# Performance work log

Measured on AMD Instinct MI355X. Metric: run time of the kernel, lower is better.

The kernel has to match this reference:

```python
import jax, jax.numpy as jnp
import numpy as np

B, T, C, H = 4, 1024, 1024, 16
D = C // H


def setup_inputs() -> dict:
    key = jax.random.key(0)
    ks = jax.random.split(key, 6)
    s = 1.0 / np.sqrt(C)
    return {
        "x": jax.random.normal(ks[0], (B, T, C), jnp.float32),
        "W_qkv": jax.random.normal(ks[1], (C, 3 * C), jnp.float32) * s,
        "b_qkv": jnp.zeros((3 * C,), jnp.float32),
        "W_out": jax.random.normal(ks[2], (C, C), jnp.float32) * s,
        "b_out": jnp.zeros((C,), jnp.float32),
        "w_sur": jax.random.normal(ks[3], (C,), jnp.float32) * s,
        "b_sur": jnp.zeros((), jnp.float32),
        "threshold": jnp.float32(0.5),
    }


def _expmap0_split(u):
    # geoopt Lorentz (k=1) expmap0: first coordinate is the time axis.
    # Minkowski norm of tangent u: sqrt(clamp(-u0^2 + |u_rest|^2, 1e-8))
    mink = -u[..., :1] ** 2 + jnp.sum(u[..., 1:] ** 2, axis=-1, keepdims=True)
    nomin = jnp.sqrt(jnp.maximum(mink, 1e-8))  # [..., 1]
    time = jnp.cosh(nomin)                      # [..., 1]
    space = jnp.sinh(nomin) * u[..., 1:] / nomin  # [..., D-1]
    return time, space


def reference(x, W_qkv, b_qkv, W_out, b_out, w_sur, b_sur, threshold):
    Bx, Tx, Cx = x.shape
    # spiking gate on query rows (causal tril over a (T,1) matrix is all-True -> no-op)
    importance = jax.nn.sigmoid(jnp.einsum("btc,c->bt", x, w_sur) + b_sur)  # [B,T]
    spikes = (importance > threshold).astype(x.dtype)                       # [B,T]
    spike_mask = spikes[:, None, :, None]                                   # [B,1,T,1]

    qkv = x @ W_qkv + b_qkv                                                 # [B,T,3C]
    qkv = qkv.reshape(Bx, Tx, 3, H, D).transpose(2, 0, 3, 1, 4)             # [3,B,H,T,D]
    q, k, v = qkv[0], qkv[1], qkv[2]

    tq, sq = _expmap0_split(q)  # [B,H,T,1], [B,H,T,D-1]
    tk, sk = _expmap0_split(k)
    # -<x,y>_L = tq*tk - <sq,sk>  (pairwise, via matmuls instead of broadcast tensors)
    neg_inner = jnp.einsum("bhie,bhje->bhij", tq, tk) - jnp.einsum(
        "bhid,bhjd->bhij", sq, sk
    )  # [B,H,T,T]
    dist = jnp.arccosh(jnp.maximum(neg_inner, 1.0 + 1e-7))
    scores = -(dist ** 2) / np.sqrt(D)

    causal = jnp.tril(jnp.ones((Tx, Tx), dtype=bool))
    scores = jnp.where(causal[None, None], scores, -jnp.inf)
    attn = jax.nn.softmax(scores, axis=-1) * spike_mask                     # [B,H,T,T]

    y = jnp.einsum("bhij,bhjd->bhid", attn, v)                              # [B,H,T,D]
    y = y.transpose(0, 2, 1, 3).reshape(Bx, Tx, Cx)
    return y @ W_out + b_out
```

## Files before the change

### kernel.cpp

```cpp
#include <hip/hip_runtime.h>
#include <math.h>

#define BB 4
#define TT 1024
#define CC 1024
#define HH 16
#define DD 64
#define NQKV (3 * CC)
#define MROWS (BB * TT)

typedef __attribute__((ext_vector_type(8))) short bf16x8;
typedef __attribute__((ext_vector_type(4))) float f32x4;

struct alignas(8) US4 { unsigned short x, y, z, w; };

__device__ __forceinline__ float b2f(unsigned short u) {
  unsigned int w = ((unsigned int)u) << 16;
  float f; __builtin_memcpy(&f, &w, 4); return f;
}
__device__ __forceinline__ unsigned short f2b(float f) {
  unsigned int u; __builtin_memcpy(&u, &f, 4);
  u += 0x7FFFu + ((u >> 16) & 1);
  return (unsigned short)(u >> 16);
}

__device__ __forceinline__ float hw_log2(float x) {
  return __builtin_amdgcn_logf(x);
}
__device__ __forceinline__ float hw_exp2(float x) {
  return __builtin_amdgcn_exp2f(x);
}

__device__ __forceinline__ void gload16(const void* g, void* l) {
  __builtin_amdgcn_global_load_lds(
      (const __attribute__((address_space(1))) unsigned int*)g,
      (__attribute__((address_space(3))) unsigned int*)l, 16, 0, 0);
}

__device__ __forceinline__ bf16x8 ld_sw(const unsigned short* row_base,
                                        int lc, int rsw) {
  return *(const bf16x8*)((const char*)row_base + (((lc ^ rsw) & 7) << 4));
}

__global__ __launch_bounds__(256) void prep(
    const float* __restrict__ x, const float* __restrict__ w_sur,
    const float* __restrict__ b_sur, const float* __restrict__ thr,
    const float* __restrict__ W_qkv, const float* __restrict__ W_out,
    float* __restrict__ spikes, unsigned short* __restrict__ xb,
    unsigned short* __restrict__ WqkvT, unsigned short* __restrict__ WoutT) {
  __shared__ float t[32][33];
  const int blk = blockIdx.x;

  if (blk < 4096) {
    const float* W; unsigned short* WT; int K, N, bx, by;
    if (blk < 3072) {
      W = W_qkv; WT = WqkvT; K = CC; N = NQKV;
      bx = blk % 96; by = blk / 96;
    } else {
      W = W_out; WT = WoutT; K = CC; N = CC;
      const int b2 = blk - 3072;
      bx = b2 & 31; by = b2 >> 5;
    }
    const int tx = threadIdx.x & 31, ty = threadIdx.x >> 5;
    const int k0 = by * 32, n0 = bx * 32;
#pragma unroll
    for (int i = 0; i < 32; i += 8)
      t[ty + i][tx] = W[(size_t)(k0 + ty + i) * N + n0 + tx];
    __syncthreads();
#pragma unroll
    for (int i = 0; i < 32; i += 8)
      WT[(size_t)(n0 + ty + i) * K + k0 + tx] = f2b(t[tx][ty + i]);
  } else {
    const int row = (blk - 4096) * 4 + (threadIdx.x >> 6);
    const int lane = threadIdx.x & 63;
    const float* xr = x + (size_t)row * CC;
    unsigned short* xo = xb + (size_t)row * CC;
    double acc = 0.0;
#pragma unroll
    for (int s = 0; s < 4; ++s) {
      const int idx = s * 256 + lane * 4;
      const float4 xv = *(const float4*)(xr + idx);
      const float4 wv = *(const float4*)(w_sur + idx);
      acc += (double)xv.x * (double)wv.x;
      acc += (double)xv.y * (double)wv.y;
      acc += (double)xv.z * (double)wv.z;
      acc += (double)xv.w * (double)wv.w;
      US4 o = {f2b(xv.x), f2b(xv.y), f2b(xv.z), f2b(xv.w)};
      *(US4*)(xo + idx) = o;
    }
#pragma unroll
    for (int off = 32; off > 0; off >>= 1) acc += __shfl_xor(acc, off, 64);
    if (lane == 0) {
      const float z = (float)acc + b_sur[0];
      const float imp = 1.0f / (1.0f + __expf(-z));
      spikes[row] = (imp > thr[0]) ? 1.0f : 0.0f;
    }
  }
}

__global__ __launch_bounds__(256, 3) void gemm_qkv(
    const unsigned short* __restrict__ A, const unsigned short* __restrict__ BT,
    const float* __restrict__ bias, unsigned short* __restrict__ qkvb,
    unsigned short* __restrict__ vT) {
  const int K = CC;
  __shared__ unsigned short SH[16384];
  unsigned short (*As)[64] = (unsigned short(*)[64])SH;
  unsigned short (*Bs)[64] = (unsigned short(*)[64])(SH + 8192);
  const int tid = threadIdx.x;
  const int lane = tid & 63;
  const int wave = tid >> 6;
  const int wr = wave >> 1;
  const int wc = wave & 1;
  const int m0 = blockIdx.y * 128;
  const int n0 = blockIdx.x * 128;
  const int ln15 = lane & 15;
  const int g = lane >> 4;
  const int rsw = ln15 & 7;

  const int srow = tid >> 3;
  const int schk = ((tid & 7) ^ (srow & 7)) * 8;
  const unsigned short* gA = A + (size_t)(m0 + srow) * K + schk;
  const unsigned short* gB = BT + (size_t)(n0 + srow) * K + schk;
  char* lA = (char*)SH + wave * 1024;
  char* lB = (char*)SH + 16384 + wave * 1024;

  f32x4 acc[4][4] = {};

  for (int k0 = 0; k0 < K; k0 += 64) {
    __syncthreads();
#pragma unroll
    for (int i = 0; i < 4; ++i)
      gload16(gA + k0 + (size_t)(32 * i) * K, lA + i * 4096);
#pragma unroll
    for (int i = 0; i < 4; ++i)
      gload16(gB + k0 + (size_t)(32 * i) * K, lB + i * 4096);
    __syncthreads();

#pragma unroll
    for (int c = 0; c < 2; ++c) {
      bf16x8 af[4], bfr[4];
#pragma unroll
      for (int i = 0; i < 4; ++i)
        af[i] = ld_sw(&As[wr * 64 + i * 16 + ln15][0], c * 4 + g, rsw);
#pragma unroll
      for (int j = 0; j < 4; ++j)
        bfr[j] = ld_sw(&Bs[wc * 64 + j * 16 + ln15][0], c * 4 + g, rsw);
#pragma unroll
      for (int i = 0; i < 4; ++i)
#pragma unroll
        for (int j = 0; j < 4; ++j)
          acc[i][j] = __builtin_amdgcn_mfma_f32_16x16x32_bf16(
              af[i], bfr[j], acc[i][j], 0, 0, 0);
    }
  }

  __syncthreads();
  unsigned short* scr = SH + wave * 4096;

  const int bx = blockIdx.x;
  if (bx < 16) {
    const bool isk = (bx >= 8);
#pragma unroll
    for (int i = 0; i < 4; ++i) {
#pragma unroll
      for (int r = 0; r < 4; ++r) {
        float u[4];
        float part = 0.f;
#pragma unroll
        for (int j = 0; j < 4; ++j) {
          u[j] = acc[i][j][r] + bias[n0 + wc * 64 + j * 16 + ln15];
          float sq = u[j] * u[j];
          if (j == 0 && ln15 == 0) sq = -sq;
          part += sq;
        }
#pragma unroll
        for (int off = 1; off < 16; off <<= 1)
          part += __shfl_xor(part, off, 64);
        const float nomin = sqrtf(fmaxf(part, 1e-8f));
        const float e = __expf(nomin);
        const float ei = __builtin_amdgcn_rcpf(e);
        const float tim = 0.5f * (e + ei);
        const float coef = 0.5f * (e - ei) * __builtin_amdgcn_rcpf(nomin);
        const int lrow = i * 16 + g * 4 + r;
#pragma unroll
        for (int j = 0; j < 4; ++j) {
          float o = (j == 0 && ln15 == 0) ? tim : coef * u[j];
          if (isk && !(j == 0 && ln15 == 0)) o = -o;
          const int col = j * 16 + ln15;
          const int ch = ((col >> 3) + lrow) & 7;
          scr[lrow * 64 + ch * 8 + (col & 7)] = f2b(o);
        }
      }
    }
#pragma unroll
    for (int it = 0; it < 8; ++it) {
      const int row = (lane >> 3) + 8 * it;
      const int ch = lane & 7;
      const int ph = (ch + row) & 7;
      const bf16x8 v = *(const bf16x8*)&scr[row * 64 + ph * 8];
      *(bf16x8*)&qkvb[(size_t)(m0 + wr * 64 + row) * NQKV + n0 + wc * 64 + ch * 8] = v;
    }
  } else {
#pragma unroll
    for (int i = 0; i < 4; ++i) {
#pragma unroll
      for (int j = 0; j < 4; ++j) {
        const float bb_ = bias[n0 + wc * 64 + j * 16 + ln15];
        const int drow = j * 16 + ln15;
#pragma unroll
        for (int r = 0; r < 4; ++r) {
          const int col = i * 16 + g * 4 + r;
          const int ch = ((col >> 3) + drow) & 7;
          scr[drow * 64 + ch * 8 + (col & 7)] = f2b(acc[i][j][r] + bb_);
        }
      }
    }
    const int hh = (bx - 16) * 2 + wc;
    const int mbase = m0 + wr * 64;
    const int bq = mbase >> 10;
    const int t0 = mbase & 1023;
#pragma unroll
    for (int it = 0; it < 8; ++it) {
      const int drow = (lane >> 3) + 8 * it;
      const int ch = lane & 7;
      const int ph = (ch + drow) & 7;
      const bf16x8 v = *(const bf16x8*)&scr[drow * 64 + ph * 8];
      *(bf16x8*)&vT[((size_t)(bq * HH + hh) * DD + drow) * TT + t0 + ch * 8] = v;
    }
  }
}

__global__ __launch_bounds__(256) void gemm_out(
    const unsigned short* __restrict__ A, const unsigned short* __restrict__ BT,
    const float* __restrict__ bias, float* __restrict__ C) {
  const int N = CC, K = CC;
  __shared__ unsigned short As[128][64];
  __shared__ unsigned short Bs[64][64];
  const int tid = threadIdx.x;
  const int lane = tid & 63;
  const int wave = tid >> 6;
  const int wm = wave * 32;
  const int m0 = blockIdx.y * 128;
  const int n0 = blockIdx.x * 64;
  const int ln15 = lane & 15;
  const int g = lane >> 4;
  const int rsw = ln15 & 7;

  const int srow = tid >> 3;
  const int schk = ((tid & 7) ^ (srow & 7)) * 8;
  const unsigned short* gA = A + (size_t)(m0 + srow) * K + schk;
  const unsigned short* gB = BT + (size_t)(n0 + srow) * K + schk;
  char* lA = (char*)As + wave * 1024;
  char* lB = (char*)Bs + wave * 1024;

  f32x4 acc[2][4] = {};

  for (int k0 = 0; k0 < K; k0 += 64) {
    __syncthreads();
#pragma unroll
    for (int i = 0; i < 4; ++i)
      gload16(gA + k0 + (size_t)(32 * i) * K, lA + i * 4096);
#pragma unroll
    for (int i = 0; i < 2; ++i)
      gload16(gB + k0 + (size_t)(32 * i) * K, lB + i * 4096);
    __syncthreads();

#pragma unroll
    for (int c = 0; c < 2; ++c) {
      bf16x8 af[2], bfr[4];
#pragma unroll
      for (int i = 0; i < 2; ++i)
        af[i] = ld_sw(&As[wm + i * 16 + ln15][0], c * 4 + g, rsw);
#pragma unroll
      for (int j = 0; j < 4; ++j)
        bfr[j] = ld_sw(&Bs[j * 16 + ln15][0], c * 4 + g, rsw);
#pragma unroll
      for (int i = 0; i < 2; ++i)
#pragma unroll
        for (int j = 0; j < 4; ++j)
          acc[i][j] = __builtin_amdgcn_mfma_f32_16x16x32_bf16(
              af[i], bfr[j], acc[i][j], 0, 0, 0);
    }
  }

#pragma unroll
  for (int i = 0; i < 2; ++i) {
#pragma unroll
    for (int r = 0; r < 4; ++r) {
      const int m = m0 + wm + i * 16 + g * 4 + r;
#pragma unroll
      for (int j = 0; j < 4; ++j) {
        const int n = n0 + j * 16 + ln15;
        C[(size_t)m * N + n] = acc[i][j][r] + bias[n];
      }
    }
  }
}

__global__ __launch_bounds__(512) void flash_mfma(
    const unsigned short* __restrict__ qkv, const unsigned short* __restrict__ vT,
    const float* __restrict__ spikes, unsigned short* __restrict__ y) {
  __shared__ unsigned short Ks[128][68];
  __shared__ unsigned short Vs[64][136];
  __shared__ unsigned short Ps[128][68];

  const int tid = threadIdx.x;
  const int lane = tid & 63;
  const int wave = tid >> 6;
  const int ln15 = lane & 15;
  const int g = lane >> 4;
  const int bh = blockIdx.y;
  const int itile = (bh < 32) ? ((int)gridDim.x - 1 - (int)blockIdx.x)
                              : (int)blockIdx.x;
  const int b = bh >> 4;
  const int h = bh & 15;
  const int i0 = itile * 128;
  const int band = wave * 16;
  const int htiles = itile + 1;
  const unsigned short* base = qkv + (size_t)b * TT * NQKV;
  const unsigned short* vbase = vT + (size_t)bh * DD * TT;
  const int qoff = h * DD;
  const int koff = CC + h * DD;

  const int ksn = tid >> 2;
  const int kqc = (tid & 3) * 2;
  const int vsn = tid >> 3;
  const int vqc = (tid & 7) * 2;

  bf16x8 qf[2];
  {
    const unsigned short* qp = base + (size_t)(i0 + band + ln15) * NQKV + qoff;
    qf[0] = *(const bf16x8*)(qp + g * 8);
    qf[1] = *(const bf16x8*)(qp + 32 + g * 8);
  }

  f32x4 accy[4] = {};
  float lrow[4] = {0.f, 0.f, 0.f, 0.f};

  float4 kr0, kr1, vr0, vr1;
  {
    const unsigned short* kp = base + (size_t)ksn * NQKV + koff + kqc * 8;
    const unsigned short* vp = vbase + (size_t)vsn * TT + vqc * 8;
    kr0 = *(const float4*)(kp + 0);
    kr1 = *(const float4*)(kp + 8);
    vr0 = *(const float4*)(vp + 0);
    vr1 = *(const float4*)(vp + 8);
  }

  for (int ht = 0; ht < htiles; ++ht) {
    const int j0h = ht * 128;
    __syncthreads();
    *(float4*)&Ks[ksn][kqc * 8 + 0] = kr0;
    *(float4*)&Ks[ksn][kqc * 8 + 8] = kr1;
    *(float4*)&Vs[vsn][vqc * 8 + 0] = vr0;
    *(float4*)&Vs[vsn][vqc * 8 + 8] = vr1;
    __syncthreads();

    if (ht + 1 < htiles) {
      const int j1 = j0h + 128;
      const unsigned short* kp = base + (size_t)(j1 + ksn) * NQKV + koff + kqc * 8;
      const unsigned short* vp = vbase + (size_t)vsn * TT + j1 + vqc * 8;
      kr0 = *(const float4*)(kp + 0);
      kr1 = *(const float4*)(kp + 8);
      vr0 = *(const float4*)(vp + 0);
      vr1 = *(const float4*)(vp + 8);
    }

#pragma unroll
    for (int t2 = 0; t2 < 2; ++t2) {
      const int j0 = j0h + t2 * 64;
      if (j0 > i0 + band + 15) continue;

      f32x4 sf[4];
#pragma unroll
      for (int j = 0; j < 4; ++j) {
        const bf16x8 k0 = *(const bf16x8*)&Ks[t2 * 64 + j * 16 + ln15][g * 8];
        const bf16x8 k1 = *(const bf16x8*)&Ks[t2 * 64 + j * 16 + ln15][32 + g * 8];
        f32x4 z = {};
        z = __builtin_amdgcn_mfma_f32_16x16x32_bf16(qf[0], k0, z, 0, 0, 0);
        sf[j] = __builtin_amdgcn_mfma_f32_16x16x32_bf16(qf[1], k1, z, 0, 0, 0);
      }

      float p[4][4];
      if (j0 + 63 <= i0 + band) {
#pragma unroll
        for (int j = 0; j < 4; ++j)
#pragma unroll
          for (int r = 0; r < 4; ++r) {
            const float l = hw_log2(fmaxf(sf[j][r], 1.0f));
            const float s = l + 1.0f;
            p[r][j] = hw_exp2(-0.08664339757f * s * s);
          }
      } else {
#pragma unroll
        for (int j = 0; j < 4; ++j) {
          const int gj = j0 + j * 16 + ln15;
#pragma unroll
          for (int r = 0; r < 4; ++r) {
            const int gi = i0 + band + g * 4 + r;
            float e;
            if (gj > gi) {
              e = 0.f;
            } else {
              const float l = hw_log2(fmaxf(sf[j][r], 1.0f));
              const float s = l + 1.0f;
              e = hw_exp2(-0.08664339757f * s * s);
            }
            p[r][j] = e;
          }
        }
      }
#pragma unroll
      for (int r = 0; r < 4; ++r)
        lrow[r] += (p[r][0] + p[r][1]) + (p[r][2] + p[r][3]);

#pragma unroll
      for (int r = 0; r < 4; ++r)
#pragma unroll
        for (int j = 0; j < 4; ++j)
          Ps[band + g * 4 + r][j * 16 + ln15] = f2b(p[r][j]);

      const bf16x8 pa0 = *(const bf16x8*)&Ps[band + ln15][g * 8];
      const bf16x8 pa1 = *(const bf16x8*)&Ps[band + ln15][32 + g * 8];
#pragma unroll
      for (int dt = 0; dt < 4; ++dt) {
        const bf16x8 v0 = *(const bf16x8*)&Vs[dt * 16 + ln15][t2 * 64 + g * 8];
        const bf16x8 v1 = *(const bf16x8*)&Vs[dt * 16 + ln15][t2 * 64 + 32 + g * 8];
        accy[dt] = __builtin_amdgcn_mfma_f32_16x16x32_bf16(pa0, v0, accy[dt], 0, 0, 0);
        accy[dt] = __builtin_amdgcn_mfma_f32_16x16x32_bf16(pa1, v1, accy[dt], 0, 0, 0);
      }
    }
  }

#pragma unroll
  for (int r = 0; r < 4; ++r) {
#pragma unroll
    for (int off = 1; off < 16; off <<= 1)
      lrow[r] += __shfl_xor(lrow[r], off, 64);
  }
  const int grow = b * TT + i0 + band + g * 4;
#pragma unroll
  for (int r = 0; r < 4; ++r) {
    const float spk = spikes[grow + r];
    const float scale = spk / lrow[r];
#pragma unroll
    for (int dt = 0; dt < 4; ++dt)
      y[(size_t)(grow + r) * CC + h * DD + dt * 16 + ln15] =
          f2b(accy[dt][r] * scale);
  }
}

extern "C" void kernel_launch(void* const* d_in, const int* in_sizes, int n_in,
                              void* d_out, int out_size, void* d_ws, size_t ws_size,
                              hipStream_t stream) {
  const float* x     = (const float*)d_in[0];
  const float* W_qkv = (const float*)d_in[1];
  const float* b_qkv = (const float*)d_in[2];
  const float* W_out = (const float*)d_in[3];
  const float* b_out = (const float*)d_in[4];
  const float* w_sur = (const float*)d_in[5];
  const float* b_sur = (const float*)d_in[6];
  const float* thr   = (const float*)d_in[7];
  float* out = (float*)d_out;

  char* w = (char*)d_ws;
  unsigned short* xb    = (unsigned short*)(w);
  unsigned short* qkvb  = (unsigned short*)(w + 8388608);
  unsigned short* vTb   = (unsigned short*)(w + 8388608 + 25165824);
  unsigned short* ybufb = (unsigned short*)(w + 8388608 + 25165824 + 8388608);
  unsigned short* WqkvT = (unsigned short*)(w + 8388608 + 25165824 + 2 * 8388608);
  unsigned short* WoutT = (unsigned short*)(w + 8388608 + 25165824 + 2 * 8388608 + 6291456);
  float* spikes = (float*)(w + 8388608 + 25165824 + 2 * 8388608 + 6291456 + 2097152);

  prep<<<5120, 256, 0, stream>>>(x, w_sur, b_sur, thr, W_qkv, W_out,
                                 spikes, xb, WqkvT, WoutT);

  gemm_qkv<<<dim3(NQKV / 128, MROWS / 128), 256, 0, stream>>>(
      xb, WqkvT, b_qkv, qkvb, vTb);

  flash_mfma<<<dim3(TT / 128, BB * HH), 512, 0, stream>>>(qkvb, vTb, spikes, ybufb);

  gemm_out<<<dim3(CC / 64, MROWS / 128), 256, 0, stream>>>(
      ybufb, WoutT, b_out, out);
}
```

Before: 168.4 us.

## Compact spiking query rows and run attention only on active rows

```diff
diff --git a/kernel.cpp b/kernel.cpp
--- a/kernel.cpp
+++ b/kernel.cpp
@@ -14,6 +14,8 @@
 
 struct alignas(8) US4 { unsigned short x, y, z, w; };
 
+__device__ __forceinline__ int imin(int a, int b) { return a < b ? a : b; }
+
 __device__ __forceinline__ float b2f(unsigned short u) {
   unsigned int w = ((unsigned int)u) << 16;
   float f; __builtin_memcpy(&f, &w, 4); return f;
@@ -47,7 +49,8 @@
     const float* __restrict__ b_sur, const float* __restrict__ thr,
     const float* __restrict__ W_qkv, const float* __restrict__ W_out,
     float* __restrict__ spikes, unsigned short* __restrict__ xb,
-    unsigned short* __restrict__ WqkvT, unsigned short* __restrict__ WoutT) {
+    unsigned short* __restrict__ WqkvT, unsigned short* __restrict__ WoutT,
+    unsigned short* __restrict__ ybufb) {
   __shared__ float t[32][33];
   const int blk = blockIdx.x;
 
@@ -90,12 +93,44 @@
     }
 #pragma unroll
     for (int off = 32; off > 0; off >>= 1) acc += __shfl_xor(acc, off, 64);
+    float spk = 0.f;
     if (lane == 0) {
       const float z = (float)acc + b_sur[0];
       const float imp = 1.0f / (1.0f + __expf(-z));
-      spikes[row] = (imp > thr[0]) ? 1.0f : 0.0f;
-    }
-  }
+      spk = (imp > thr[0]) ? 1.0f : 0.0f;
+      spikes[row] = spk;
+    }
+    spk = __shfl(spk, 0, 64);
+    if (spk == 0.f) {
+      unsigned short* yz = ybufb + (size_t)row * CC;
+      const bf16x8 z8 = {};
+      *(bf16x8*)&yz[lane * 16] = z8;
+      *(bf16x8*)&yz[lane * 16 + 8] = z8;
+    }
+  }
+}
+
+__global__ __launch_bounds__(1024) void compact(
+    const float* __restrict__ spikes, unsigned short* __restrict__ cidx,
+    int* __restrict__ cnt) {
+  const int b = blockIdx.x;
+  const int t = threadIdx.x;
+  const int lane = t & 63, wv = t >> 6;
+  __shared__ int wsum[16];
+  __shared__ int woff[16];
+  const bool f = spikes[b * TT + t] > 0.5f;
+  const unsigned long long bal = __ballot(f);
+  const int wpre = __popcll(bal & ((1ull << lane) - 1ull));
+  if (lane == 0) wsum[wv] = __popcll(bal);
+  __syncthreads();
+  if (t == 0) {
+    int s = 0;
+#pragma unroll
+    for (int i = 0; i < 16; ++i) { woff[i] = s; s += wsum[i]; }
+    cnt[b] = s;
+  }
+  __syncthreads();
+  if (f) cidx[b * TT + woff[wv] + wpre] = (unsigned short)t;
 }
 
 __global__ __launch_bounds__(256, 3) void gemm_qkv(
@@ -299,7 +334,8 @@
 
 __global__ __launch_bounds__(512) void flash_mfma(
     const unsigned short* __restrict__ qkv, const unsigned short* __restrict__ vT,
-    const float* __restrict__ spikes, unsigned short* __restrict__ y) {
+    const unsigned short* __restrict__ cidx, const int* __restrict__ cntp,
+    unsigned short* __restrict__ y) {
   __shared__ unsigned short Ks[128][68];
   __shared__ unsigned short Vs[64][136];
   __shared__ unsigned short Ps[128][68];
@@ -316,7 +352,13 @@
   const int h = bh & 15;
   const int i0 = itile * 128;
   const int band = wave * 16;
-  const int htiles = itile + 1;
+
+  const int cnt = cntp[b];
+  if (i0 >= cnt) return;
+
+  const int omax_blk = cidx[b * TT + imin(i0 + 127, cnt - 1)];
+  const int htiles = omax_blk / 128 + 1;
+
   const unsigned short* base = qkv + (size_t)b * TT * NQKV;
   const unsigned short* vbase = vT + (size_t)bh * DD * TT;
   const int qoff = h * DD;
@@ -327,9 +369,17 @@
   const int vsn = tid >> 3;
   const int vqc = (tid & 7) * 2;
 
+  const int qslot = imin(i0 + band + ln15, cnt - 1);
+  const int qorig = (int)cidx[b * TT + qslot];
+  int oi_[4];
+#pragma unroll
+  for (int r = 0; r < 4; ++r) oi_[r] = __shfl(qorig, g * 4 + r, 16);
+  const int obandmin = __shfl(qorig, 0, 16);
+  const int obandmax = __shfl(qorig, 15, 16);
+
   bf16x8 qf[2];
   {
-    const unsigned short* qp = base + (size_t)(i0 + band + ln15) * NQKV + qoff;
+    const unsigned short* qp = base + (size_t)qorig * NQKV + qoff;
     qf[0] = *(const bf16x8*)(qp + g * 8);
     qf[1] = *(const bf16x8*)(qp + 32 + g * 8);
   }
@@ -369,7 +419,7 @@
 #pragma unroll
     for (int t2 = 0; t2 < 2; ++t2) {
       const int j0 = j0h + t2 * 64;
-      if (j0 > i0 + band + 15) continue;
+      if (j0 > obandmax) continue;
 
       f32x4 sf[4];
 #pragma unroll
@@ -382,7 +432,7 @@
       }
 
       float p[4][4];
-      if (j0 + 63 <= i0 + band) {
+      if (j0 + 63 <= obandmin) {
 #pragma unroll
         for (int j = 0; j < 4; ++j)
 #pragma unroll
@@ -397,9 +447,8 @@
           const int gj = j0 + j * 16 + ln15;
 #pragma unroll
           for (int r = 0; r < 4; ++r) {
-            const int gi = i0 + band + g * 4 + r;
             float e;
-            if (gj > gi) {
+            if (gj > oi_[r]) {
               e = 0.f;
             } else {
               const float l = hw_log2(fmaxf(sf[j][r], 1.0f));
@@ -438,15 +487,16 @@
     for (int off = 1; off < 16; off <<= 1)
       lrow[r] += __shfl_xor(lrow[r], off, 64);
   }
-  const int grow = b * TT + i0 + band + g * 4;
 #pragma unroll
   for (int r = 0; r < 4; ++r) {
-    const float spk = spikes[grow + r];
-    const float scale = spk / lrow[r];
-#pragma unroll
-    for (int dt = 0; dt < 4; ++dt)
-      y[(size_t)(grow + r) * CC + h * DD + dt * 16 + ln15] =
-          f2b(accy[dt][r] * scale);
+    const int slot = i0 + band + g * 4 + r;
+    if (slot < cnt) {
+      const float scale = 1.0f / lrow[r];
+      const size_t yrow = (size_t)(b * TT + oi_[r]);
+#pragma unroll
+      for (int dt = 0; dt < 4; ++dt)
+        y[yrow * CC + h * DD + dt * 16 + ln15] = f2b(accy[dt][r] * scale);
+    }
   }
 }
 
@@ -470,15 +520,19 @@
   unsigned short* ybufb = (unsigned short*)(w + 8388608 + 25165824 + 8388608);
   unsigned short* WqkvT = (unsigned short*)(w + 8388608 + 25165824 + 2 * 8388608);
   unsigned short* WoutT = (unsigned short*)(w + 8388608 + 25165824 + 2 * 8388608 + 6291456);
-  float* spikes = (float*)(w + 8388608 + 25165824 + 2 * 8388608 + 6291456 + 2097152);
+  float* spikes = (float*)(w + 58720256);
+  unsigned short* cidx = (unsigned short*)(w + 58720256 + 16384);
+  int* cnt = (int*)(w + 58720256 + 16384 + 8192);
 
   prep<<<5120, 256, 0, stream>>>(x, w_sur, b_sur, thr, W_qkv, W_out,
-                                 spikes, xb, WqkvT, WoutT);
+                                 spikes, xb, WqkvT, WoutT, ybufb);
+
+  compact<<<4, 1024, 0, stream>>>(spikes, cidx, cnt);
 
   gemm_qkv<<<dim3(NQKV / 128, MROWS / 128), 256, 0, stream>>>(
       xb, WqkvT, b_qkv, qkvb, vTb);
 
-  flash_mfma<<<dim3(TT / 128, BB * HH), 512, 0, stream>>>(qkvb, vTb, spikes, ybufb);
+  flash_mfma<<<dim3(TT / 128, BB * HH), 512, 0, stream>>>(qkvb, vTb, cidx, cnt, ybufb);
 
   gemm_out<<<dim3(CC / 64, MROWS / 128), 256, 0, stream>>>(
       ybufb, WoutT, b_out, out);
```

Result: slower. 180.7 us (+7.3%).

## Enlarge QKV GEMM tile to 256x256 with double-buffered LDS prefetch

Applied to the files above, without the earlier changes.

```diff
diff --git a/kernel.cpp b/kernel.cpp
--- a/kernel.cpp
+++ b/kernel.cpp
@@ -98,21 +98,19 @@
   }
 }
 
-__global__ __launch_bounds__(256, 3) void gemm_qkv(
+__global__ __launch_bounds__(512, 2) void gemm_qkv(
     const unsigned short* __restrict__ A, const unsigned short* __restrict__ BT,
     const float* __restrict__ bias, unsigned short* __restrict__ qkvb,
     unsigned short* __restrict__ vT) {
   const int K = CC;
-  __shared__ unsigned short SH[16384];
-  unsigned short (*As)[64] = (unsigned short(*)[64])SH;
-  unsigned short (*Bs)[64] = (unsigned short(*)[64])(SH + 8192);
+  __shared__ unsigned short SH[65536];
   const int tid = threadIdx.x;
   const int lane = tid & 63;
   const int wave = tid >> 6;
-  const int wr = wave >> 1;
-  const int wc = wave & 1;
-  const int m0 = blockIdx.y * 128;
-  const int n0 = blockIdx.x * 128;
+  const int wr = wave >> 2;
+  const int wc = wave & 3;
+  const int m0 = blockIdx.y * 256;
+  const int n0 = blockIdx.x * 256;
   const int ln15 = lane & 15;
   const int g = lane >> 4;
   const int rsw = ln15 & 7;
@@ -121,47 +119,79 @@
   const int schk = ((tid & 7) ^ (srow & 7)) * 8;
   const unsigned short* gA = A + (size_t)(m0 + srow) * K + schk;
   const unsigned short* gB = BT + (size_t)(n0 + srow) * K + schk;
-  char* lA = (char*)SH + wave * 1024;
-  char* lB = (char*)SH + 16384 + wave * 1024;
-
-  f32x4 acc[4][4] = {};
-
-  for (int k0 = 0; k0 < K; k0 += 64) {
+  char* lbase = (char*)SH;
+  const int wave1k = wave * 1024;
+
+  f32x4 acc[8][4] = {};
+
+#pragma unroll
+  for (int g64 = 0; g64 < 4; ++g64)
+    gload16(gA + (size_t)(g64 * 64) * K, lbase + g64 * 8192 + wave1k);
+#pragma unroll
+  for (int g64 = 0; g64 < 4; ++g64)
+    gload16(gB + (size_t)(g64 * 64) * K, lbase + 65536 + g64 * 8192 + wave1k);
+  __syncthreads();
+
+  for (int kt = 0; kt < 16; ++kt) {
+    const unsigned short* As = SH + (kt & 1) * 16384;
+    const unsigned short* Bs = SH + 32768 + (kt & 1) * 16384;
+    const int nd = (kt + 1) & 1;
+    const bool more = (kt + 1 < 16);
+    const int kc = (kt + 1) * 64;
+
+    bf16x8 bfr[4][2];
+#pragma unroll
+    for (int p = 0; p < 4; ++p) {
+      if (p == 0 && more) {
+#pragma unroll
+        for (int g64 = 0; g64 < 4; ++g64)
+          gload16(gA + (size_t)(g64 * 64) * K + kc,
+                  lbase + nd * 32768 + g64 * 8192 + wave1k);
+      }
+      if (p == 1 && more) {
+#pragma unroll
+        for (int g64 = 0; g64 < 4; ++g64)
+          gload16(gB + (size_t)(g64 * 64) * K + kc,
+                  lbase + 65536 + nd * 32768 + g64 * 8192 + wave1k);
+      }
+      if (p == 0) {
+#pragma unroll
+        for (int j = 0; j < 4; ++j)
+#pragma unroll
+          for (int c = 0; c < 2; ++c)
+            bfr[j][c] = ld_sw(Bs + (wc * 64 + j * 16 + ln15) * 64, c * 4 + g, rsw);
+      }
+      bf16x8 af[2][2];
+#pragma unroll
+      for (int ii = 0; ii < 2; ++ii)
+#pragma unroll
+        for (int c = 0; c < 2; ++c)
+          af[ii][c] = ld_sw(As + (wr * 128 + (p * 2 + ii) * 16 + ln15) * 64,
+                            c * 4 + g, rsw);
+
+      __builtin_amdgcn_s_setprio(1);
+#pragma unroll
+      for (int ii = 0; ii < 2; ++ii)
+#pragma unroll
+        for (int j = 0; j < 4; ++j)
+#pragma unroll
+          for (int c = 0; c < 2; ++c)
+            acc[p * 2 + ii][j] = __builtin_amdgcn_mfma_f32_16x16x32_bf16(
+                af[ii][c], bfr[j][c], acc[p * 2 + ii][j], 0, 0, 0);
+      __builtin_amdgcn_s_setprio(0);
+      __builtin_amdgcn_sched_barrier(0);
+      __builtin_amdgcn_s_barrier();
+    }
     __syncthreads();
-#pragma unroll
-    for (int i = 0; i < 4; ++i)
-      gload16(gA + k0 + (size_t)(32 * i) * K, lA + i * 4096);
-#pragma unroll
-    for (int i = 0; i < 4; ++i)
-      gload16(gB + k0 + (size_t)(32 * i) * K, lB + i * 4096);
-    __syncthreads();
-
-#pragma unroll
-    for (int c = 0; c < 2; ++c) {
-      bf16x8 af[4], bfr[4];
-#pragma unroll
-      for (int i = 0; i < 4; ++i)
-        af[i] = ld_sw(&As[wr * 64 + i * 16 + ln15][0], c * 4 + g, rsw);
-#pragma unroll
-      for (int j = 0; j < 4; ++j)
-        bfr[j] = ld_sw(&Bs[wc * 64 + j * 16 + ln15][0], c * 4 + g, rsw);
-#pragma unroll
-      for (int i = 0; i < 4; ++i)
-#pragma unroll
-        for (int j = 0; j < 4; ++j)
-          acc[i][j] = __builtin_amdgcn_mfma_f32_16x16x32_bf16(
-              af[i], bfr[j], acc[i][j], 0, 0, 0);
-    }
-  }
-
-  __syncthreads();
-  unsigned short* scr = SH + wave * 4096;
+  }
+
+  unsigned short* scr = SH + wave * 8192;
 
   const int bx = blockIdx.x;
-  if (bx < 16) {
-    const bool isk = (bx >= 8);
-#pragma unroll
-    for (int i = 0; i < 4; ++i) {
+  if (bx < 8) {
+    const bool isk = (bx >= 4);
+#pragma unroll
+    for (int i = 0; i < 8; ++i) {
 #pragma unroll
       for (int r = 0; r < 4; ++r) {
         float u[4];
@@ -193,16 +223,16 @@
       }
     }
 #pragma unroll
-    for (int it = 0; it < 8; ++it) {
+    for (int it = 0; it < 16; ++it) {
       const int row = (lane >> 3) + 8 * it;
       const int ch = lane & 7;
       const int ph = (ch + row) & 7;
       const bf16x8 v = *(const bf16x8*)&scr[row * 64 + ph * 8];
-      *(bf16x8*)&qkvb[(size_t)(m0 + wr * 64 + row) * NQKV + n0 + wc * 64 + ch * 8] = v;
+      *(bf16x8*)&qkvb[(size_t)(m0 + wr * 128 + row) * NQKV + n0 + wc * 64 + ch * 8] = v;
     }
   } else {
 #pragma unroll
-    for (int i = 0; i < 4; ++i) {
+    for (int i = 0; i < 8; ++i) {
 #pragma unroll
       for (int j = 0; j < 4; ++j) {
         const float bb_ = bias[n0 + wc * 64 + j * 16 + ln15];
@@ -210,22 +240,22 @@
 #pragma unroll
         for (int r = 0; r < 4; ++r) {
           const int col = i * 16 + g * 4 + r;
-          const int ch = ((col >> 3) + drow) & 7;
-          scr[drow * 64 + ch * 8 + (col & 7)] = f2b(acc[i][j][r] + bb_);
+          const int ch = ((col >> 3) + drow) & 15;
+          scr[drow * 128 + ch * 8 + (col & 7)] = f2b(acc[i][j][r] + bb_);
         }
       }
     }
-    const int hh = (bx - 16) * 2 + wc;
-    const int mbase = m0 + wr * 64;
+    const int hh = (bx - 8) * 4 + wc;
+    const int mbase = m0 + wr * 128;
     const int bq = mbase >> 10;
     const int t0 = mbase & 1023;
 #pragma unroll
-    for (int it = 0; it < 8; ++it) {
-      const int drow = (lane >> 3) + 8 * it;
-      const int ch = lane & 7;
-      const int ph = (ch + drow) & 7;
-      const bf16x8 v = *(const bf16x8*)&scr[drow * 64 + ph * 8];
-      *(bf16x8*)&vT[((size_t)(bq * HH + hh) * DD + drow) * TT + t0 + ch * 8] = v;
+    for (int it = 0; it < 16; ++it) {
+      const int drow = (lane >> 4) + 4 * it;
+      const int chunk = lane & 15;
+      const int ph = (chunk + drow) & 15;
+      const bf16x8 v = *(const bf16x8*)&scr[drow * 128 + ph * 8];
+      *(bf16x8*)&vT[((size_t)(bq * HH + hh) * DD + drow) * TT + t0 + chunk * 8] = v;
     }
   }
 }
@@ -475,7 +505,7 @@
   prep<<<5120, 256, 0, stream>>>(x, w_sur, b_sur, thr, W_qkv, W_out,
                                  spikes, xb, WqkvT, WoutT);
 
-  gemm_qkv<<<dim3(NQKV / 128, MROWS / 128), 256, 0, stream>>>(
+  gemm_qkv<<<dim3(NQKV / 256, MROWS / 256), 512, 0, stream>>>(
       xb, WqkvT, b_qkv, qkvb, vTb);
 
   flash_mfma<<<dim3(TT / 128, BB * HH), 512, 0, stream>>>(qkvb, vTb, spikes, ybufb);
```

New measurement: 173.6 us. 3.1% more time.
